# Performance work log

Hardware: AMD Instinct MI355X
Metric: run time of the kernel (lower is better)

The kernel has to match this reference:

```python
import jax, jax.numpy as jnp
import numpy as np
import math

LS1 = [0, 1, 2]
LS2 = [0, 1, 2]
B = 1048576


def _fact(n):
    return math.factorial(n)


def _w3j_complex(j1, j2, j3, m1, m2, m3):
    # Racah formula for the complex-basis Wigner 3j symbol.
    if m1 + m2 + m3 != 0:
        return 0.0
    if not (abs(j1 - j2) <= j3 <= j1 + j2):
        return 0.0
    if abs(m1) > j1 or abs(m2) > j2 or abs(m3) > j3:
        return 0.0
    tmin = max(0, j2 - j3 - m1, j1 - j3 + m2)
    tmax = min(j1 + j2 - j3, j1 - m1, j2 + m2)
    s = 0.0
    for t in range(tmin, tmax + 1):
        s += (-1) ** t / (
            _fact(t) * _fact(j3 - j2 + t + m1) * _fact(j3 - j1 + t - m2)
            * _fact(j1 + j2 - j3 - t) * _fact(j1 - t - m1) * _fact(j2 - t + m2)
        )
    delta = math.sqrt(
        _fact(j1 + j2 - j3) * _fact(j1 - j2 + j3) * _fact(-j1 + j2 + j3)
        / _fact(j1 + j2 + j3 + 1)
    )
    pref = math.sqrt(
        _fact(j1 + m1) * _fact(j1 - m1) * _fact(j2 + m2) * _fact(j2 - m2)
        * _fact(j3 + m3) * _fact(j3 - m3)
    )
    return ((-1) ** (j1 - j2 - m3)) * delta * pref * s


def _U(l):
    # Unitary change of basis: complex spherical harmonics -> real spherical harmonics.
    d = 2 * l + 1
    U = np.zeros((d, d), dtype=complex)
    s = 1.0 / math.sqrt(2.0)
    for m in range(-l, l + 1):
        i = m + l
        if m > 0:
            U[i, m + l] = ((-1) ** m) * s
            U[i, -m + l] = s
        elif m == 0:
            U[i, l] = 1.0
        else:
            a = -m
            U[i, m + l] = 1j * s
            U[i, a + l] = -1j * ((-1) ** a) * s
    return U


def _real_w3j(l1, l2, l3):
    # Wigner 3j tensor in the real spherical-harmonic basis, Frobenius norm 1.
    W = np.zeros((2 * l1 + 1, 2 * l2 + 1, 2 * l3 + 1), dtype=complex)
    for m1 in range(-l1, l1 + 1):
        for m2 in range(-l2, l2 + 1):
            for m3 in range(-l3, l3 + 1):
                W[m1 + l1, m2 + l2, m3 + l3] = _w3j_complex(l1, l2, l3, m1, m2, m3)
    T = np.einsum('am,bn,co,mno->abc', _U(l1), _U(l2), _U(l3), W)
    re, im = T.real, T.imag
    T = re if np.abs(re).sum() >= np.abs(im).sum() else im
    return T.astype(np.float32)


def build_cb_matrix(ls1, ls2):
    # Faithful replication of EinsumTensorProduct.__init__ layout logic.
    layout = {}
    cb_height = 0
    idx1 = 0
    for l1 in ls1:
        idx2 = 0
        for l2 in ls2:
            for l3 in range(abs(l1 - l2), l1 + l2 + 1):
                layout.setdefault(l3, []).append((l1, l2, idx1, idx2))
                cb_height += 2 * l3 + 1
            idx2 += 2 * l2 + 1
        idx1 += 2 * l1 + 1
    dim1 = sum(2 * l + 1 for l in ls1)
    dim2 = sum(2 * l + 1 for l in ls2)
    cb = np.zeros((cb_height, dim1, dim2), dtype=np.float32)
    lmax2 = max(ls2)
    row = 0
    for l3 in sorted(layout.keys()):
        mults = sorted(layout[l3], key=lambda x: x[0] * lmax2 + x[1])
        for l1, l2, o1, o2 in mults:
            blk = _real_w3j(l1, l2, l3) * math.sqrt(2 * l3 + 1)  # [m1, m2, m3]
            cb[row:row + 2 * l3 + 1, o1:o1 + 2 * l1 + 1, o2:o2 + 2 * l2 + 1] = \
                np.transpose(blk, (2, 0, 1))
            row += 2 * l3 + 1
    return cb


def setup_inputs() -> dict:
    key = jax.random.key(0)
    k1, k2 = jax.random.split(key)
    dim1 = sum(2 * l + 1 for l in LS1)
    dim2 = sum(2 * l + 1 for l in LS2)
    cb = jnp.asarray(build_cb_matrix(LS1, LS2))  # [81, 9, 9]
    in1 = jax.random.normal(k1, (B, dim1), dtype=jnp.float32)
    in2 = jax.random.normal(k2, (B, dim2), dtype=jnp.float32)
    return {"in1": in1, "in2": in2, "cb_matrix": cb}


def reference(in1, in2, cb_matrix):
    # out[b, k] = sum_{i,j} in1[b, i] * in2[b, j] * cb[k, i, j]
    return jnp.einsum('bi,bj,kij->bk', in1, in2, cb_matrix)
```

## Files before the change

### kernel.cpp

```cpp
#include <hip/hip_runtime.h>
#include <stdint.h>

#define THREADS 192
#define DIM 9
#define NK 81
#define F 81
#define NCHUNK 6
#define TILE 32
#define GRID 1280

typedef __attribute__((ext_vector_type(8))) short short8;
typedef __attribute__((ext_vector_type(16))) float f32x16;
typedef __attribute__((ext_vector_type(4))) float f32x4;

__device__ inline unsigned short f32_bf16(float x) {
    unsigned u = __float_as_uint(x);
    u += 0x7FFFu + ((u >> 16) & 1u);
    return (unsigned short)(u >> 16);
}
__device__ inline float bf16_f32(unsigned short h) {
    return __uint_as_float(((unsigned)h) << 16);
}

__global__ __launch_bounds__(THREADS, 4)
void tp_mfma(const float* __restrict__ in1, const float* __restrict__ in2,
             const float* __restrict__ cb, float* __restrict__ out,
             int nrows, int ntiles) {
    __shared__ __attribute__((aligned(16))) float s_in[3][2][576];
    __shared__ __attribute__((aligned(16))) float s_c[TILE * NK];

    const int tid  = threadIdx.x;
    const int lane = tid & 63;
    const int wave = tid >> 6;
    const int l31  = lane & 31;
    const int h    = lane >> 5;
    const int kcol = 32 * wave + l31;

    short8 Bhi[NCHUNK], Blo[NCHUNK];
    for (int c = 0; c < NCHUNK; ++c) {
        union { short8 v; unsigned short u[8]; } bh, bl;
        for (int j = 0; j < 8; ++j) {
            int f = c * 16 + h * 8 + j;
            float v = 0.0f;
            if (f < F && kcol < NK) v = cb[kcol * F + f];
            unsigned short hb = f32_bf16(v);
            bh.u[j] = hb;
            bl.u[j] = f32_bf16(v - bf16_f32(hb));
        }
        Bhi[c] = bh.v; Blo[c] = bl.v;
    }

    const unsigned lim16 = (unsigned)nrows * 36u - 16u;
    const unsigned lim4  = (unsigned)nrows * 36u - 4u;
    const uintptr_t p1 = (uintptr_t)in1;
    const uintptr_t p2 = (uintptr_t)in2;

    auto stage = [&](int t, int buf) {
        const unsigned tb = (unsigned)t * 1152u;
        float* dst0 = &s_in[wave][buf][0];
        {   unsigned o = tb + (unsigned)lane * 16u;
            if (o > lim16) o = lim16;
            __builtin_amdgcn_global_load_lds(
                (__attribute__((address_space(1))) void*)(p1 + o),
                (__attribute__((address_space(3))) void*)dst0, 16, 0, 0);
        }
        {   unsigned bb = 1024u + (unsigned)lane * 16u;
            unsigned o1 = tb + bb;          if (o1 > lim16) o1 = lim16;
            unsigned o2 = tb + bb - 1152u;  if (o2 > lim16) o2 = lim16;
            uintptr_t src = (bb < 1152u) ? (p1 + o1) : (p2 + o2);
            __builtin_amdgcn_global_load_lds(
                (__attribute__((address_space(1))) void*)src,
                (__attribute__((address_space(3))) void*)(dst0 + 256), 16, 0, 0);
        }
        {   unsigned o = tb + 896u + (unsigned)lane * 4u;
            if (o > lim4) o = lim4;
            __builtin_amdgcn_global_load_lds(
                (__attribute__((address_space(1))) void*)(p2 + o),
                (__attribute__((address_space(3))) void*)(dst0 + 512), 4, 0, 0);
        }
    };

    int cur = 0;
    const int t0 = blockIdx.x;
    if (t0 < ntiles) stage(t0, 0);

    for (int t = t0; t < ntiles; t += gridDim.x) {
        const int tn = t + gridDim.x;
        const bool hasn = (tn < ntiles);
        if (hasn) stage(tn, cur ^ 1);

        if (t == t0) {
            if (hasn) asm volatile("s_waitcnt vmcnt(3)" ::: "memory");
            else      asm volatile("s_waitcnt vmcnt(0)" ::: "memory");
        } else {
            if (hasn) asm volatile("s_waitcnt vmcnt(7)" ::: "memory");
            else      asm volatile("s_waitcnt vmcnt(4)" ::: "memory");
        }
        __builtin_amdgcn_sched_barrier(0);

        const float* sa = &s_in[wave][cur][0];
        float a[DIM], b[DIM];
#pragma unroll
        for (int i = 0; i < DIM; ++i) {
            a[i] = sa[l31 * 9 + i];
            b[i] = sa[288 + l31 * 9 + i];
        }

        short8 A[NCHUNK];
#pragma unroll
        for (int c = 0; c < NCHUNK; ++c) {
            union { short8 v; unsigned short u[8]; } av;
#pragma unroll
            for (int j = 0; j < 8; ++j) {
                const int f0 = c * 16 + j;
                const int f1 = f0 + 8;
                float q0 = (f0 < F) ? a[f0 / 9] * b[f0 % 9] : 0.0f;
                float q1 = (f1 < F) ? a[f1 / 9] * b[f1 % 9] : 0.0f;
                av.u[j] = f32_bf16(h ? q1 : q0);
            }
            A[c] = av.v;
        }

        f32x16 acc = {0.f,0.f,0.f,0.f, 0.f,0.f,0.f,0.f, 0.f,0.f,0.f,0.f, 0.f,0.f,0.f,0.f};
#pragma unroll
        for (int c = 0; c < NCHUNK; ++c) {
            acc = __builtin_amdgcn_mfma_f32_32x32x16_bf16(A[c], Bhi[c], acc, 0, 0, 0);
            acc = __builtin_amdgcn_mfma_f32_32x32x16_bf16(A[c], Blo[c], acc, 0, 0, 0);
        }

        if (kcol < NK) {
#pragma unroll
            for (int r = 0; r < 16; ++r) {
                const int mrow = (r & 3) + 8 * (r >> 2) + 4 * h;
                s_c[mrow * NK + kcol] = acc[r];
            }
        }
        asm volatile("s_waitcnt lgkmcnt(0)\ns_barrier" ::: "memory");

        const long r0 = (long)t * TILE;
        if (r0 + TILE <= (long)nrows) {
            const f32x4* sc4 = (const f32x4*)s_c;
            f32x4* o4 = (f32x4*)(out + r0 * NK);
#pragma unroll
            for (int q = 0; q < 4; ++q) {
                int idx = tid + q * THREADS;
                int idc = (idx >= 648) ? idx - 648 : idx;
                o4[idc] = sc4[idc];
            }
        } else {
            for (int e = tid; e < TILE * NK; e += THREADS) {
                long g = r0 * NK + e;
                if (g < (long)nrows * NK) out[g] = s_c[e];
            }
        }
        asm volatile("s_barrier" ::: "memory");
        cur ^= 1;
    }
}

extern "C" void kernel_launch(void* const* d_in, const int* in_sizes, int n_in,
                              void* d_out, int out_size, void* d_ws, size_t ws_size,
                              hipStream_t stream) {
    const float* in1 = (const float*)d_in[0];
    const float* in2 = (const float*)d_in[1];
    const float* cb  = (const float*)d_in[2];
    float* out = (float*)d_out;

    int nrows  = in_sizes[0] / DIM;
    int ntiles = (nrows + TILE - 1) / TILE;
    int grid = (GRID < ntiles) ? GRID : ntiles;

    tp_mfma<<<grid, THREADS, 0, stream>>>(in1, in2, cb, out, nrows, ntiles);
}
```

Baseline: 412.5 us.

## Share input staging across waves, double-buffer output LDS, drop trailing barrier

The per-wave input staging buffers become one shared double buffer, which cuts LDS use. The output staging buffer is now double-buffered, so the trailing barrier at the end of each iteration can go. A/B products are converted to bf16 with the packed v_cvt_pk_bf16_f32 instruction, and the hi and lo MFMA chains use separate accumulators so they no longer depend on each other. The grid grows to 1536 blocks. The risk is correctness: all three waves now issue global_load_lds into the same buffer, so each wave's data must land where the others expect it, and the race margin across iterations is thinner without the barrier.

```diff
diff --git a/kernel.cpp b/kernel.cpp
--- a/kernel.cpp
+++ b/kernel.cpp
@@ -7,7 +7,7 @@
 #define F 81
 #define NCHUNK 6
 #define TILE 32
-#define GRID 1280
+#define GRID 1536
 
 typedef __attribute__((ext_vector_type(8))) short short8;
 typedef __attribute__((ext_vector_type(16))) float f32x16;
@@ -26,8 +26,8 @@
 void tp_mfma(const float* __restrict__ in1, const float* __restrict__ in2,
              const float* __restrict__ cb, float* __restrict__ out,
              int nrows, int ntiles) {
-    __shared__ __attribute__((aligned(16))) float s_in[3][2][576];
-    __shared__ __attribute__((aligned(16))) float s_c[TILE * NK];
+    __shared__ __attribute__((aligned(16))) float s_in[2][576];
+    __shared__ __attribute__((aligned(16))) float s_c[2][TILE * NK];
 
     const int tid  = threadIdx.x;
     const int lane = tid & 63;
@@ -57,7 +57,7 @@
 
     auto stage = [&](int t, int buf) {
         const unsigned tb = (unsigned)t * 1152u;
-        float* dst0 = &s_in[wave][buf][0];
+        float* dst0 = &s_in[buf][0];
         {   unsigned o = tb + (unsigned)lane * 16u;
             if (o > lim16) o = lim16;
             __builtin_amdgcn_global_load_lds(
@@ -98,7 +98,7 @@
         }
         __builtin_amdgcn_sched_barrier(0);
 
-        const float* sa = &s_in[wave][cur][0];
+        const float* sa = &s_in[cur][0];
         float a[DIM], b[DIM];
 #pragma unroll
         for (int i = 0; i < DIM; ++i) {
@@ -109,37 +109,49 @@
         short8 A[NCHUNK];
 #pragma unroll
         for (int c = 0; c < NCHUNK; ++c) {
-            union { short8 v; unsigned short u[8]; } av;
+            union { short8 v; unsigned d[4]; } av;
 #pragma unroll
-            for (int j = 0; j < 8; ++j) {
-                const int f0 = c * 16 + j;
-                const int f1 = f0 + 8;
-                float q0 = (f0 < F) ? a[f0 / 9] * b[f0 % 9] : 0.0f;
-                float q1 = (f1 < F) ? a[f1 / 9] * b[f1 % 9] : 0.0f;
-                av.u[j] = f32_bf16(h ? q1 : q0);
+            for (int k = 0; k < 4; ++k) {
+                float vlo, vhi;
+                {
+                    const int f0 = c * 16 + 2 * k, f1 = f0 + 8;
+                    float q0 = (f0 < F) ? a[f0 / 9] * b[f0 % 9] : 0.0f;
+                    float q1 = (f1 < F) ? a[f1 / 9] * b[f1 % 9] : 0.0f;
+                    vlo = h ? q1 : q0;
+                }
+                {
+                    const int f0 = c * 16 + 2 * k + 1, f1 = f0 + 8;
+                    float q0 = (f0 < F) ? a[f0 / 9] * b[f0 % 9] : 0.0f;
+                    float q1 = (f1 < F) ? a[f1 / 9] * b[f1 % 9] : 0.0f;
+                    vhi = h ? q1 : q0;
+                }
+                unsigned dw;
+                asm("v_cvt_pk_bf16_f32 %0, %1, %2" : "=v"(dw) : "v"(vlo), "v"(vhi));
+                av.d[k] = dw;
             }
             A[c] = av.v;
         }
 
-        f32x16 acc = {0.f,0.f,0.f,0.f, 0.f,0.f,0.f,0.f, 0.f,0.f,0.f,0.f, 0.f,0.f,0.f,0.f};
+        f32x16 acch = {0.f,0.f,0.f,0.f, 0.f,0.f,0.f,0.f, 0.f,0.f,0.f,0.f, 0.f,0.f,0.f,0.f};
+        f32x16 accl = acch;
 #pragma unroll
         for (int c = 0; c < NCHUNK; ++c) {
-            acc = __builtin_amdgcn_mfma_f32_32x32x16_bf16(A[c], Bhi[c], acc, 0, 0, 0);
-            acc = __builtin_amdgcn_mfma_f32_32x32x16_bf16(A[c], Blo[c], acc, 0, 0, 0);
+            acch = __builtin_amdgcn_mfma_f32_32x32x16_bf16(A[c], Bhi[c], acch, 0, 0, 0);
+            accl = __builtin_amdgcn_mfma_f32_32x32x16_bf16(A[c], Blo[c], accl, 0, 0, 0);
         }
 
         if (kcol < NK) {
 #pragma unroll
             for (int r = 0; r < 16; ++r) {
                 const int mrow = (r & 3) + 8 * (r >> 2) + 4 * h;
-                s_c[mrow * NK + kcol] = acc[r];
+                s_c[cur][mrow * NK + kcol] = acch[r] + accl[r];
             }
         }
         asm volatile("s_waitcnt lgkmcnt(0)\ns_barrier" ::: "memory");
 
         const long r0 = (long)t * TILE;
         if (r0 + TILE <= (long)nrows) {
-            const f32x4* sc4 = (const f32x4*)s_c;
+            const f32x4* sc4 = (const f32x4*)&s_c[cur][0];
             f32x4* o4 = (f32x4*)(out + r0 * NK);
 #pragma unroll
             for (int q = 0; q < 4; ++q) {
@@ -150,10 +162,9 @@
         } else {
             for (int e = tid; e < TILE * NK; e += THREADS) {
                 long g = r0 * NK + e;
-                if (g < (long)nrows * NK) out[g] = s_c[e];
+                if (g < (long)nrows * NK) out[g] = s_c[cur][e];
             }
         }
-        asm volatile("s_barrier" ::: "memory");
         cur ^= 1;
     }
 }
```

New measurement: 427.0 us. 1.04x slower.
